# Performance work log

Measured on AMD Instinct MI355X. Metric: run time of the kernel, lower is better.

The kernel has to match this reference:

```python
import jax, jax.numpy as jnp
import numpy as np

N = 100000
E = 3200000
IN_DIM, HID, MLP_HID, K = 3, 64, 128, 15


def setup_inputs() -> dict:
    key = jax.random.key(0)
    ks = jax.random.split(key, 10)
    x = jax.random.normal(ks[0], (N, IN_DIM), dtype=jnp.float32)
    edge_index = jax.random.randint(ks[1], (2, E), 0, N, dtype=jnp.int32)
    def glorot(k, shape):
        lim = float(np.sqrt(6.0 / (shape[0] + shape[1])))
        return jax.random.uniform(k, shape, jnp.float32, -lim, lim)
    return {
        "x": x,
        "edge_index": edge_index,
        "W1": glorot(ks[2], (IN_DIM, HID)), "b1": jnp.zeros((HID,), jnp.float32),
        "W2": glorot(ks[3], (HID, HID)),    "b2": jnp.zeros((HID,), jnp.float32),
        "Wm1": glorot(ks[4], (HID, MLP_HID)), "bm1": jnp.zeros((MLP_HID,), jnp.float32),
        "Wm2": glorot(ks[5], (MLP_HID, K)),   "bm2": jnp.zeros((K,), jnp.float32),
    }


def _gcn_layer(h, W, b, src, dst, deg_inv_sqrt, n):
    # h: [N, Fin] -> [N, Fout]; GCNConv: D^-1/2 (A+I) D^-1/2 (h W) + b
    hw = h @ W  # dense GEMM first (Fin small)
    norm = deg_inv_sqrt[src] * deg_inv_sqrt[dst]  # [E+N]
    msg = hw[src] * norm[:, None]                 # irregular gather, [E+N, Fout]
    out = jax.ops.segment_sum(msg, dst, num_segments=n)  # scatter-add
    return out + b


def reference(x, edge_index, W1, b1, W2, b2, Wm1, bm1, Wm2, bm2):
    n = x.shape[0]
    loops = jnp.arange(n, dtype=edge_index.dtype)
    src = jnp.concatenate([edge_index[0], loops])  # self-loops appended
    dst = jnp.concatenate([edge_index[1], loops])
    deg = jax.ops.segment_sum(jnp.ones_like(dst, dtype=x.dtype), dst, num_segments=n)
    deg_inv_sqrt = jnp.where(deg > 0, jax.lax.rsqrt(jnp.maximum(deg, 1.0)), 0.0)

    h = jax.nn.elu(_gcn_layer(x, W1, b1, src, dst, deg_inv_sqrt, n))
    h = jax.nn.elu(_gcn_layer(h, W2, b2, src, dst, deg_inv_sqrt, n))
    # MLP (dropout is identity in eval mode)
    h = jax.nn.elu(h @ Wm1 + bm1)
    H = h @ Wm2 + bm2
    return jax.nn.softmax(H, axis=1)  # [N, K]
```

## Files before the change

### kernel.cpp

```cpp
#include <hip/hip_runtime.h>
#include <hip/hip_fp16.h>
#include <math.h>


#define SPAN 128
#define CAP  4608
#define CH   4096
#define EPT  16
#define H2P  88
#define MSP2 136

typedef _Float16 v8hf __attribute__((ext_vector_type(8)));
typedef float    v4f  __attribute__((ext_vector_type(4)));

__device__ __forceinline__ float elu(float v) { return v > 0.f ? v : expm1f(v); }

__global__ __launch_bounds__(256) void prep_kernel(const float* __restrict__ W2,
    const float* __restrict__ Wm1, __half* __restrict__ W2t, __half* __restrict__ Wm1t,
    int* __restrict__ cursor, int NBK) {
    int tid = blockIdx.x * 256 + threadIdx.x;
    if (tid < NBK) cursor[tid] = 0;
    if (tid < 64 * 64) {
        int f = tid >> 6, k = tid & 63;
        W2t[f * 64 + k] = __float2half(W2[k * 64 + f]);
    }
    if (tid < 128 * 64) {
        int j = tid >> 6, f = tid & 63;
        Wm1t[j * 64 + f] = __float2half(Wm1[f * 128 + j]);
    }
}

__global__ __launch_bounds__(256) void scatter_kernel(const int* __restrict__ src,
    const int* __restrict__ dst, int* __restrict__ cursor, unsigned* __restrict__ colb,
    int E, int NBK) {
    __shared__ int hist[1024];
    __shared__ unsigned gb[1024];
    int tid = threadIdx.x;
    int chunk = blockIdx.x;
    for (int i = tid; i < NBK; i += 256) hist[i] = 0;
    __syncthreads();
    int base = chunk * CH;
    int cnt = min(CH, E - base);
    unsigned br[EPT], dt[EPT];
#pragma unroll
    for (int j = 0; j < EPT; ++j) {
        int idx = j * 256 + tid;
        br[j] = 0xFFFFFFFFu;
        if (idx < cnt) {
            int e = base + idx;
            int s = src[e], d = dst[e];
            int b = d >> 7;
            int r = atomicAdd(&hist[b], 1);
            br[j] = ((unsigned)b << 13) | (unsigned)r;
            dt[j] = ((unsigned)(d & 127) << 17) | (unsigned)s;
        }
    }
    __syncthreads();
    for (int b = tid; b < NBK; b += 256) {
        int c = hist[b];
        gb[b] = (unsigned)(b * CAP) + (c ? (unsigned)atomicAdd(&cursor[b], c) : 0u);
    }
    __syncthreads();
#pragma unroll
    for (int j = 0; j < EPT; ++j) {
        if (br[j] != 0xFFFFFFFFu) {
            int b = br[j] >> 13;
            int r = br[j] & 8191;
            unsigned pos = gb[b] + (unsigned)r;
            if (pos < (unsigned)(b + 1) * CAP) colb[pos] = dt[j];
        }
    }
}

__global__ __launch_bounds__(256) void csr_sort_kernel(const unsigned* __restrict__ colb,
    const int* __restrict__ cursor, const float* __restrict__ x,
    int* __restrict__ row_ptr, int* __restrict__ col,
    float* __restrict__ dis, __half* __restrict__ sxh, int N, int NBK) {
    __shared__ unsigned ebuf[CAP];
    __shared__ int sbuf[CAP];
    __shared__ int cnt[SPAN], pref[SPAN], fill[SPAN];
    __shared__ int redbuf[256];
    int b = blockIdx.x, tid = threadIdx.x;
    int n = min(cursor[b], CAP);
    int base = b * CAP;
    int partial = 0;
    for (int i2 = tid; i2 < b; i2 += 256) partial += min(cursor[i2], CAP);
    redbuf[tid] = partial;
    if (tid < SPAN) cnt[tid] = 0;
    for (int i = tid; i < n; i += 256) ebuf[i] = colb[base + i];
    __syncthreads();
    for (int off = 128; off; off >>= 1) {
        if (tid < off) redbuf[tid] += redbuf[tid + off];
        __syncthreads();
    }
    int bb = redbuf[0];
    for (int i = tid; i < n; i += 256) atomicAdd(&cnt[(ebuf[i] >> 17) & 127], 1);
    __syncthreads();
    if (tid < SPAN) pref[tid] = cnt[tid];
    __syncthreads();
    for (int off = 1; off < SPAN; off <<= 1) {
        int xv = (tid < SPAN && tid >= off) ? pref[tid - off] : 0;
        __syncthreads();
        if (tid < SPAN) pref[tid] += xv;
        __syncthreads();
    }
    if (tid < SPAN) {
        int ex = pref[tid] - cnt[tid];
        fill[tid] = ex;
        int node = b * SPAN + tid;
        if (node < N) {
            row_ptr[node] = bb + ex;
            float r = rsqrtf((float)(cnt[tid] + 1));
            dis[node] = r;
            __half2 h0 = __floats2half2_rn(r * x[node * 3 + 0], r * x[node * 3 + 1]);
            __half2 h1 = __floats2half2_rn(r * x[node * 3 + 2], 0.f);
            uint2 w; w.x = *(unsigned*)&h0; w.y = *(unsigned*)&h1;
            *(uint2*)(sxh + (size_t)node * 4) = w;
        }
    }
    if (b == NBK - 1 && tid == 0) row_ptr[N] = bb + n;
    __syncthreads();
    for (int i = tid; i < n; i += 256) {
        unsigned e = ebuf[i];
        int pos = atomicAdd(&fill[(e >> 17) & 127], 1);
        sbuf[pos] = (int)(e & 0x1FFFF);
    }
    __syncthreads();
    for (int i = tid; i < n; i += 256) col[bb + i] = sbuf[i];
}

__global__ void agg3_kernel(const __half* __restrict__ sxh, const int* __restrict__ row_ptr,
                            const int* __restrict__ col, const float* __restrict__ dis,
                            const float* __restrict__ W1, const float* __restrict__ b1,
                            __half* __restrict__ s1h, int N) {
    int wave = (blockIdx.x * blockDim.x + threadIdx.x) >> 6;
    int lane = threadIdx.x & 63;
    if (wave >= N) return;
    int d = wave;
    int start = row_ptr[d], end = row_ptr[d + 1];
    float a0 = 0.f, a1 = 0.f, a2v = 0.f;
    for (int i = start + lane; i < end; i += 64) {
        uint2 rq = *(const uint2*)(sxh + (size_t)col[i] * 4);
        float2 u0 = __half22float2(*(__half2*)&rq.x);
        float2 u1 = __half22float2(*(__half2*)&rq.y);
        a0 += u0.x; a1 += u0.y; a2v += u1.x;
    }
#pragma unroll
    for (int off = 32; off; off >>= 1) {
        a0  += __shfl_xor(a0, off);
        a1  += __shfl_xor(a1, off);
        a2v += __shfl_xor(a2v, off);
    }
    {
        uint2 rq = *(const uint2*)(sxh + (size_t)d * 4);
        float2 u0 = __half22float2(*(__half2*)&rq.x);
        float2 u1 = __half22float2(*(__half2*)&rq.y);
        a0 += u0.x; a1 += u0.y; a2v += u1.x;
    }
    float r = dis[d];
    float v = r * (a0 * W1[lane] + a1 * W1[64 + lane] + a2v * W1[128 + lane]) + b1[lane];
    s1h[(size_t)d * 64 + lane] = __float2half(r * elu(v));
}

__global__ void agg64_kernel(const __half* __restrict__ s1h, const int* __restrict__ row_ptr,
                             const int* __restrict__ col, const float* __restrict__ dis,
                             __half* __restrict__ a2h, int N) {
    int wave = (blockIdx.x * blockDim.x + threadIdx.x) >> 6;
    int lane = threadIdx.x & 63;
    int hl = lane & 31;
    int sub = hl >> 4;
    int fl  = hl & 15;
    int d = wave * 2 + (lane >> 5);
    bool act = d < N;
    int start = 0, end = 0;
    if (act) { start = row_ptr[d]; end = row_ptr[d + 1]; }
    float ax = 0.f, ay = 0.f, az = 0.f, aw = 0.f;
    int i = start;
    for (; i + 7 < end; i += 8) {
#pragma unroll
        for (int qq = 0; qq < 2; ++qq) {
            int c0 = col[i + 4 * qq + sub];
            int c1 = col[i + 4 * qq + 2 + sub];
            uint2 r0 = *(const uint2*)(s1h + (size_t)c0 * 64 + fl * 4);
            uint2 r1 = *(const uint2*)(s1h + (size_t)c1 * 64 + fl * 4);
            __half2 p0 = __hadd2(*(__half2*)&r0.x, *(__half2*)&r1.x);
            __half2 p1 = __hadd2(*(__half2*)&r0.y, *(__half2*)&r1.y);
            float2 u0 = __half22float2(p0);
            float2 u1 = __half22float2(p1);
            ax += u0.x; ay += u0.y; az += u1.x; aw += u1.y;
        }
    }
    for (; i < end; ++i) {
        if (sub == 0) {
            uint2 r0 = *(const uint2*)(s1h + (size_t)col[i] * 64 + fl * 4);
            float2 u0 = __half22float2(*(__half2*)&r0.x);
            float2 u1 = __half22float2(*(__half2*)&r0.y);
            ax += u0.x; ay += u0.y; az += u1.x; aw += u1.y;
        }
    }
    ax += __shfl_xor(ax, 16);
    ay += __shfl_xor(ay, 16);
    az += __shfl_xor(az, 16);
    aw += __shfl_xor(aw, 16);
    if (act && sub == 0) {
        uint2 r0 = *(const uint2*)(s1h + (size_t)d * 64 + fl * 4);
        float2 u0 = __half22float2(*(__half2*)&r0.x);
        float2 u1 = __half22float2(*(__half2*)&r0.y);
        float rd = dis[d];
        __half2 o0 = __floats2half2_rn(rd * (ax + u0.x), rd * (ay + u0.y));
        __half2 o1 = __floats2half2_rn(rd * (az + u1.x), rd * (aw + u1.y));
        uint2 w; w.x = *(unsigned*)&o0; w.y = *(unsigned*)&o1;
        *(uint2*)(a2h + (size_t)d * 64 + fl * 4) = w;
    }
}

__global__ __launch_bounds__(256) void h1_kernel(const __half* __restrict__ a2h,
    const __half* __restrict__ W2t, const float* __restrict__ b2g,
    const __half* __restrict__ Wm1t, const float* __restrict__ bm1g,
    const float* __restrict__ Wm2g, const float* __restrict__ bm2g,
    float* __restrict__ out, int N) {
    __shared__ __align__(16) __half h2s[64 * H2P];
    __shared__ __align__(16) __half ms[64 * MSP2];
    __shared__ float Wt2[128 * 16];
    __shared__ float lgs[16 * 16];
    __shared__ float b2s[64], bm1s[128], bm2s[16];
    int tid = threadIdx.x;
    if (tid < 64)  b2s[tid]  = b2g[tid];
    if (tid < 128) bm1s[tid] = bm1g[tid];
    if (tid < 16)  bm2s[tid] = (tid < 15) ? bm2g[tid] : 0.f;
    for (int i = tid; i < 128 * 16; i += 256) {
        int j = i >> 4, c = i & 15;
        Wt2[i] = (c < 15) ? Wm2g[j * 15 + c] : 0.f;
    }
    __syncthreads();

    int wave = tid >> 6, lane = tid & 63;
    int q = lane >> 4, l16 = lane & 15;
    int base = blockIdx.x * 64;

    {
        int nodeRow = base + wave * 16 + l16;
        size_t arow = (size_t)min(nodeRow, N - 1) * 64;
        v8hf af0 = *(const v8hf*)(a2h + arow + q * 8);
        v8hf af1 = *(const v8hf*)(a2h + arow + 32 + q * 8);
#pragma unroll
        for (int fb = 0; fb < 4; ++fb) {
            float bb = b2s[fb * 16 + l16];
            v4f acc = {bb, bb, bb, bb};
            v8hf b0 = *(const v8hf*)(W2t + (fb * 16 + l16) * 64 + q * 8);
            v8hf b1 = *(const v8hf*)(W2t + (fb * 16 + l16) * 64 + 32 + q * 8);
            acc = __builtin_amdgcn_mfma_f32_16x16x32_f16(af0, b0, acc, 0, 0, 0);
            acc = __builtin_amdgcn_mfma_f32_16x16x32_f16(af1, b1, acc, 0, 0, 0);
#pragma unroll
            for (int r = 0; r < 4; ++r)
                h2s[(wave * 16 + q * 4 + r) * H2P + fb * 16 + l16] =
                    __float2half(elu(acc[r]));
        }
    }
    __syncthreads();
    {
        int arow = (wave * 16 + l16) * H2P;
        v8hf af0 = *(const v8hf*)(h2s + arow + q * 8);
        v8hf af1 = *(const v8hf*)(h2s + arow + 32 + q * 8);
#pragma unroll
        for (int jb = 0; jb < 8; ++jb) {
            float bb = bm1s[jb * 16 + l16];
            v4f acc = {bb, bb, bb, bb};
            v8hf b0 = *(const v8hf*)(Wm1t + (jb * 16 + l16) * 64 + q * 8);
            v8hf b1 = *(const v8hf*)(Wm1t + (jb * 16 + l16) * 64 + 32 + q * 8);
            acc = __builtin_amdgcn_mfma_f32_16x16x32_f16(af0, b0, acc, 0, 0, 0);
            acc = __builtin_amdgcn_mfma_f32_16x16x32_f16(af1, b1, acc, 0, 0, 0);
#pragma unroll
            for (int r = 0; r < 4; ++r)
                ms[(wave * 16 + q * 4 + r) * MSP2 + jb * 16 + l16] =
                    __float2half(elu(acc[r]));
        }
    }
    __syncthreads();
    {
        int cc = tid % 15;
        int nn = tid / 15;
        bool actC = tid < 240;
#pragma unroll
        for (int it = 0; it < 4; ++it) {
            if (actC) {
                int row = it * 16 + nn;
                float acc = bm2s[cc];
                const __half2* mrow = (const __half2*)(ms + row * MSP2);
#pragma unroll 4
                for (int j2 = 0; j2 < 64; ++j2) {
                    float2 u = __half22float2(mrow[j2]);
                    acc = fmaf(u.x, Wt2[(2 * j2) * 16 + cc],
                          fmaf(u.y, Wt2[(2 * j2 + 1) * 16 + cc], acc));
                }
                lgs[nn * 16 + cc] = acc;
            }
            __syncthreads();
            if (actC) {
                int node = base + it * 16 + nn;
                float mx = lgs[nn * 16 + 0];
#pragma unroll
                for (int c2 = 1; c2 < 15; ++c2) mx = fmaxf(mx, lgs[nn * 16 + c2]);
                float sden = 0.f;
#pragma unroll
                for (int c2 = 0; c2 < 15; ++c2) sden += __expf(lgs[nn * 16 + c2] - mx);
                if (node < N)
                    out[(size_t)node * 15 + cc] = __expf(lgs[nn * 16 + cc] - mx) / sden;
            }
            __syncthreads();
        }
    }
}

extern "C" void kernel_launch(void* const* d_in, const int* in_sizes, int n_in,
                              void* d_out, int out_size, void* d_ws, size_t ws_size,
                              hipStream_t stream) {
    const float* x   = (const float*)d_in[0];
    const int*   ei  = (const int*)d_in[1];
    const float* W1  = (const float*)d_in[2];
    const float* b1  = (const float*)d_in[3];
    const float* W2  = (const float*)d_in[4];
    const float* b2  = (const float*)d_in[5];
    const float* Wm1 = (const float*)d_in[6];
    const float* bm1 = (const float*)d_in[7];
    const float* Wm2 = (const float*)d_in[8];
    const float* bm2 = (const float*)d_in[9];
    float* out = (float*)d_out;

    int N = in_sizes[0] / 3;
    int E = in_sizes[1] / 2;
    const int* src = ei;
    const int* dst = ei + E;
    int NBK = (N + SPAN - 1) / SPAN;

    uintptr_t p = (uintptr_t)d_ws;
    auto carve = [&](size_t bytes) -> void* {
        p = (p + 255) & ~(uintptr_t)255;
        void* r = (void*)p;
        p += bytes;
        return r;
    };
    __half*   a2h     = (__half*)carve((size_t)N * 64 * 2);
    __half*   s1h     = (__half*)carve((size_t)N * 64 * 2);
    int*      cursor  = (int*)carve((size_t)NBK * 4);
    int*      row_ptr = (int*)carve((size_t)(N + 1) * 4);
    float*    dis     = (float*)carve((size_t)N * 4);
    __half*   sxh     = (__half*)carve((size_t)N * 8);
    int*      col     = (int*)carve((size_t)E * 4);
    __half*   W2t     = (__half*)carve(64 * 64 * 2);
    __half*   Wm1t    = (__half*)carve(128 * 64 * 2);
    unsigned* colb = (unsigned*)a2h;

    int nChunks = (E + CH - 1) / CH;
    int waveBlocks3  = (N + 3) / 4;
    int waveBlocks64 = (N + 7) / 8;
    int nTiles = (N + 63) / 64;
    prep_kernel<<<32, 256, 0, stream>>>(W2, Wm1, W2t, Wm1t, cursor, NBK);
    scatter_kernel<<<nChunks, 256, 0, stream>>>(src, dst, cursor, colb, E, NBK);
    csr_sort_kernel<<<NBK, 256, 0, stream>>>(colb, cursor, x, row_ptr, col, dis, sxh, N, NBK);
    agg3_kernel<<<waveBlocks3, 256, 0, stream>>>(sxh, row_ptr, col, dis, W1, b1, s1h, N);
    agg64_kernel<<<waveBlocks64, 256, 0, stream>>>(s1h, row_ptr, col, dis, a2h, N);
    h1_kernel<<<nTiles, 256, 0, stream>>>(a2h, W2t, b2, Wm1t, bm1, Wm2, bm2, out, N);
}
```

Baseline: 279.6 us.

## Rework agg64 gather to half2-per-lane with eight accumulators, shuffle-based softmax

The 64-feature aggregation now has each 32-lane half-wave cover one node with a half2 per lane. It issues eight independent neighbour-row loads per iteration into separate fp32 accumulators, replacing the earlier split-edge scheme with fp16 pairwise adds and a cross-lane reduction. The MLP output stage computes softmax with 16-lane shuffle reductions instead of a shared-memory logits buffer and two barriers per iteration. The scatter chunk size and edges-per-thread are also doubled. The aim is more memory-level parallelism in the gather and fewer syncs, at the cost of narrower 4-byte loads and higher register use.

```diff
diff --git a/kernel.cpp b/kernel.cpp
--- a/kernel.cpp
+++ b/kernel.cpp
@@ -5,8 +5,8 @@
 
 #define SPAN 128
 #define CAP  4608
-#define CH   4096
-#define EPT  16
+#define CH   8192
+#define EPT  32
 #define H2P  88
 #define MSP2 136
 
@@ -162,55 +162,50 @@
     s1h[(size_t)d * 64 + lane] = __float2half(r * elu(v));
 }
 
-__global__ void agg64_kernel(const __half* __restrict__ s1h, const int* __restrict__ row_ptr,
+__global__ void agg64_kernel(const __half2* __restrict__ s1h, const int* __restrict__ row_ptr,
                              const int* __restrict__ col, const float* __restrict__ dis,
-                             __half* __restrict__ a2h, int N) {
+                             __half2* __restrict__ a2h, int N) {
     int wave = (blockIdx.x * blockDim.x + threadIdx.x) >> 6;
     int lane = threadIdx.x & 63;
     int hl = lane & 31;
-    int sub = hl >> 4;
-    int fl  = hl & 15;
     int d = wave * 2 + (lane >> 5);
     bool act = d < N;
     int start = 0, end = 0;
     if (act) { start = row_ptr[d]; end = row_ptr[d + 1]; }
-    float ax = 0.f, ay = 0.f, az = 0.f, aw = 0.f;
+    float a0x = 0.f, a0y = 0.f, a1x = 0.f, a1y = 0.f;
+    float a2x = 0.f, a2y = 0.f, a3x = 0.f, a3y = 0.f;
+    float a4x = 0.f, a4y = 0.f, a5x = 0.f, a5y = 0.f;
+    float a6x = 0.f, a6y = 0.f, a7x = 0.f, a7y = 0.f;
+    if (act) {
+        float2 v = __half22float2(s1h[(size_t)d * 32 + hl]);
+        a0x = v.x; a0y = v.y;
+    }
     int i = start;
     for (; i + 7 < end; i += 8) {
-#pragma unroll
-        for (int qq = 0; qq < 2; ++qq) {
-            int c0 = col[i + 4 * qq + sub];
-            int c1 = col[i + 4 * qq + 2 + sub];
-            uint2 r0 = *(const uint2*)(s1h + (size_t)c0 * 64 + fl * 4);
-            uint2 r1 = *(const uint2*)(s1h + (size_t)c1 * 64 + fl * 4);
-            __half2 p0 = __hadd2(*(__half2*)&r0.x, *(__half2*)&r1.x);
-            __half2 p1 = __hadd2(*(__half2*)&r0.y, *(__half2*)&r1.y);
-            float2 u0 = __half22float2(p0);
-            float2 u1 = __half22float2(p1);
-            ax += u0.x; ay += u0.y; az += u1.x; aw += u1.y;
-        }
+        int c0 = col[i],     c1 = col[i + 1], c2 = col[i + 2], c3 = col[i + 3];
+        int c4 = col[i + 4], c5 = col[i + 5], c6 = col[i + 6], c7 = col[i + 7];
+        float2 v0 = __half22float2(s1h[(size_t)c0 * 32 + hl]);
+        float2 v1 = __half22float2(s1h[(size_t)c1 * 32 + hl]);
+        float2 v2 = __half22float2(s1h[(size_t)c2 * 32 + hl]);
+        float2 v3 = __half22float2(s1h[(size_t)c3 * 32 + hl]);
+        float2 v4 = __half22float2(s1h[(size_t)c4 * 32 + hl]);
+        float2 v5 = __half22float2(s1h[(size_t)c5 * 32 + hl]);
+        float2 v6 = __half22float2(s1h[(size_t)c6 * 32 + hl]);
+        float2 v7 = __half22float2(s1h[(size_t)c7 * 32 + hl]);
+        a0x += v0.x; a0y += v0.y; a1x += v1.x; a1y += v1.y;
+        a2x += v2.x; a2y += v2.y; a3x += v3.x; a3y += v3.y;
+        a4x += v4.x; a4y += v4.y; a5x += v5.x; a5y += v5.y;
+        a6x += v6.x; a6y += v6.y; a7x += v7.x; a7y += v7.y;
     }
     for (; i < end; ++i) {
-        if (sub == 0) {
-            uint2 r0 = *(const uint2*)(s1h + (size_t)col[i] * 64 + fl * 4);
-            float2 u0 = __half22float2(*(__half2*)&r0.x);
-            float2 u1 = __half22float2(*(__half2*)&r0.y);
-            ax += u0.x; ay += u0.y; az += u1.x; aw += u1.y;
-        }
-    }
-    ax += __shfl_xor(ax, 16);
-    ay += __shfl_xor(ay, 16);
-    az += __shfl_xor(az, 16);
-    aw += __shfl_xor(aw, 16);
-    if (act && sub == 0) {
-        uint2 r0 = *(const uint2*)(s1h + (size_t)d * 64 + fl * 4);
-        float2 u0 = __half22float2(*(__half2*)&r0.x);
-        float2 u1 = __half22float2(*(__half2*)&r0.y);
-        float rd = dis[d];
-        __half2 o0 = __floats2half2_rn(rd * (ax + u0.x), rd * (ay + u0.y));
-        __half2 o1 = __floats2half2_rn(rd * (az + u1.x), rd * (aw + u1.y));
-        uint2 w; w.x = *(unsigned*)&o0; w.y = *(unsigned*)&o1;
-        *(uint2*)(a2h + (size_t)d * 64 + fl * 4) = w;
+        float2 v = __half22float2(s1h[(size_t)col[i] * 32 + hl]);
+        a0x += v.x; a0y += v.y;
+    }
+    if (act) {
+        float r = dis[d];
+        float ox = r * (((a0x + a1x) + (a2x + a3x)) + ((a4x + a5x) + (a6x + a7x)));
+        float oy = r * (((a0y + a1y) + (a2y + a3y)) + ((a4y + a5y) + (a6y + a7y)));
+        a2h[(size_t)d * 32 + hl] = __floats2half2_rn(ox, oy);
     }
 }
 
@@ -222,7 +217,6 @@
     __shared__ __align__(16) __half h2s[64 * H2P];
     __shared__ __align__(16) __half ms[64 * MSP2];
     __shared__ float Wt2[128 * 16];
-    __shared__ float lgs[16 * 16];
     __shared__ float b2s[64], bm1s[128], bm2s[16];
     int tid = threadIdx.x;
     if (tid < 64)  b2s[tid]  = b2g[tid];
@@ -278,36 +272,34 @@
     }
     __syncthreads();
     {
-        int cc = tid % 15;
-        int nn = tid / 15;
-        bool actC = tid < 240;
+        int c = l16;
+        int nloc = wave * 4 + q;
 #pragma unroll
         for (int it = 0; it < 4; ++it) {
-            if (actC) {
-                int row = it * 16 + nn;
-                float acc = bm2s[cc];
-                const __half2* mrow = (const __half2*)(ms + row * MSP2);
+            int row = it * 16 + nloc;
+            float acc = bm2s[c];
+            const __half2* mrow = (const __half2*)(ms + row * MSP2);
 #pragma unroll 4
-                for (int j2 = 0; j2 < 64; ++j2) {
-                    float2 u = __half22float2(mrow[j2]);
-                    acc = fmaf(u.x, Wt2[(2 * j2) * 16 + cc],
-                          fmaf(u.y, Wt2[(2 * j2 + 1) * 16 + cc], acc));
-                }
-                lgs[nn * 16 + cc] = acc;
+            for (int j2 = 0; j2 < 64; ++j2) {
+                float2 u = __half22float2(mrow[j2]);
+                acc = fmaf(u.x, Wt2[(2 * j2) * 16 + c],
+                      fmaf(u.y, Wt2[(2 * j2 + 1) * 16 + c], acc));
             }
-            __syncthreads();
-            if (actC) {
-                int node = base + it * 16 + nn;
-                float mx = lgs[nn * 16 + 0];
-#pragma unroll
-                for (int c2 = 1; c2 < 15; ++c2) mx = fmaxf(mx, lgs[nn * 16 + c2]);
-                float sden = 0.f;
-#pragma unroll
-                for (int c2 = 0; c2 < 15; ++c2) sden += __expf(lgs[nn * 16 + c2] - mx);
-                if (node < N)
-                    out[(size_t)node * 15 + cc] = __expf(lgs[nn * 16 + cc] - mx) / sden;
-            }
-            __syncthreads();
+            float lg = (c < 15) ? acc : -1e30f;
+            float mx = lg;
+            mx = fmaxf(mx, __shfl_xor(mx, 1));
+            mx = fmaxf(mx, __shfl_xor(mx, 2));
+            mx = fmaxf(mx, __shfl_xor(mx, 4));
+            mx = fmaxf(mx, __shfl_xor(mx, 8));
+            float ex = (c < 15) ? __expf(lg - mx) : 0.f;
+            float sden = ex;
+            sden += __shfl_xor(sden, 1);
+            sden += __shfl_xor(sden, 2);
+            sden += __shfl_xor(sden, 4);
+            sden += __shfl_xor(sden, 8);
+            int node = base + row;
+            if (c < 15 && node < N)
+                out[(size_t)node * 15 + c] = ex / sden;
         }
     }
 }
@@ -359,6 +351,7 @@
     scatter_kernel<<<nChunks, 256, 0, stream>>>(src, dst, cursor, colb, E, NBK);
     csr_sort_kernel<<<NBK, 256, 0, stream>>>(colb, cursor, x, row_ptr, col, dis, sxh, N, NBK);
     agg3_kernel<<<waveBlocks3, 256, 0, stream>>>(sxh, row_ptr, col, dis, W1, b1, s1h, N);
-    agg64_kernel<<<waveBlocks64, 256, 0, stream>>>(s1h, row_ptr, col, dis, a2h, N);
+    agg64_kernel<<<waveBlocks64, 256, 0, stream>>>((const __half2*)s1h, row_ptr, col, dis,
+                                                   (__half2*)a2h, N);
     h1_kernel<<<nTiles, 256, 0, stream>>>(a2h, W2t, b2, Wm1t, bm1, Wm2, bm2, out, N);
 }
```

Result: faster. 267.9 us (-4.2%).
